# Performance work log

Measured on AMD Instinct MI355X. Metric: run time of the kernel, lower is better.

The kernel has to match this reference:

```python
import jax, jax.numpy as jnp
import numpy as np

BS, N, W, R = 32, 2048, 128, 8
EPS = 1e-8

def setup_inputs() -> dict:
    key = jax.random.key(0)
    ks = jax.random.split(key, 16)
    memory = jax.random.normal(ks[0], (N, W), jnp.float32)
    usage_vector = jax.random.uniform(ks[1], (BS, N), jnp.float32)
    p = jax.random.uniform(ks[2], (BS, N), jnp.float32)
    precedence_weighting = p / p.sum(1, keepdims=True)
    temporal_memory_linkage = jax.random.uniform(ks[3], (BS, N, N), jnp.float32) / N
    lr = jax.random.uniform(ks[4], (BS, N, R), jnp.float32)
    last_read_weightings = lr / lr.sum(1, keepdims=True)
    read_keys = jax.random.normal(ks[5], (BS, W, R), jnp.float32)
    read_strengths = 1.0 + 4.0 * jax.random.uniform(ks[6], (BS, R), jnp.float32)
    write_key = jax.random.normal(ks[7], (BS, W), jnp.float32)
    write_strength = 1.0 + 4.0 * jax.random.uniform(ks[8], (BS, 1), jnp.float32)
    erase_vector = jax.random.uniform(ks[9], (BS, W), jnp.float32)
    write_vector = jax.random.normal(ks[10], (BS, W), jnp.float32)
    free_gates = jax.random.uniform(ks[11], (BS, R), jnp.float32)
    allocation_gate = jax.random.uniform(ks[12], (BS, 1), jnp.float32)
    write_gate = jax.random.uniform(ks[13], (BS, 1), jnp.float32)
    rm = jax.random.uniform(ks[14], (BS, R, 3), jnp.float32)
    read_modes = rm / rm.sum(-1, keepdims=True)
    return dict(memory=memory, usage_vector=usage_vector,
                precedence_weighting=precedence_weighting,
                temporal_memory_linkage=temporal_memory_linkage,
                last_read_weightings=last_read_weightings,
                read_keys=read_keys, read_strengths=read_strengths,
                write_key=write_key, write_strength=write_strength,
                erase_vector=erase_vector, write_vector=write_vector,
                free_gates=free_gates, allocation_gate=allocation_gate,
                write_gate=write_gate, read_modes=read_modes)


def reference(memory, usage_vector, precedence_weighting, temporal_memory_linkage,
              last_read_weightings, read_keys, read_strengths, write_key,
              write_strength, erase_vector, write_vector, free_gates,
              allocation_gate, write_gate, read_modes):
    bs = usage_vector.shape[0]
    # --- allocation weighting (sort + cumprod + gather), from previous usage ---
    sorted_u = jnp.sort(usage_vector, axis=1)                 # (bs,N)
    indices = jnp.argsort(usage_vector, axis=1)               # (bs,N)
    cp = jnp.cumprod(sorted_u, axis=1)
    cp = jnp.concatenate([jnp.ones((bs, 1), usage_vector.dtype), cp], axis=1)[:, :-1]
    alloc_sorted = (1.0 - sorted_u) * cp
    # faithful to torch.gather(aw, 1, indices)
    alloc = jnp.take_along_axis(alloc_sorted, indices, axis=1)  # (bs,N)
    # --- write content weighting (cosine sim + softmax) ---
    innerprod = write_key @ memory.T                          # (bs,N)
    memnorm = jnp.linalg.norm(memory, axis=1)                 # (N,)
    writenorm = jnp.linalg.norm(write_key, axis=1)            # (bs,)
    sim = innerprod / jnp.clip(memnorm[None, :] * writenorm[:, None], EPS)
    cw = jax.nn.softmax(sim * write_strength, axis=1)         # (bs,N)
    # --- write weighting ---
    ww = write_gate * (allocation_gate * alloc + (1.0 - allocation_gate) * cw)  # (bs,N)
    # --- memory retention + usage update ---
    psi = jnp.prod(1.0 - last_read_weightings * free_gates[:, None, :], axis=2)  # (bs,N)
    usage_new = (usage_vector + ww - usage_vector * ww) * psi
    # --- write to memory (erase then add, mean over batch) ---
    erase_outer = ww[:, :, None] * erase_vector[:, None, :]   # (bs,N,W)
    add_outer = ww[:, :, None] * write_vector[:, None, :]     # (bs,N,W)
    memory_new = jnp.mean(memory[None] * (1.0 - erase_outer) + add_outer, axis=0)  # (N,W)
    # --- temporal linkage update (uses previous precedence) ---
    ww_i = ww[:, :, None]                                     # (bs,N,1)
    ww_j = ww[:, None, :]                                     # (bs,1,N)
    L_new = (1.0 - ww_j - ww_i) * temporal_memory_linkage + ww_i * precedence_weighting[:, None, :]
    # --- precedence update ---
    prec_new = (1.0 - ww.sum(1, keepdims=True)) * precedence_weighting + ww
    # --- forward / backward weightings ---
    bw = jnp.matmul(L_new, last_read_weightings)              # (bs,N,R)
    fw = jnp.matmul(jnp.swapaxes(L_new, 1, 2), last_read_weightings)  # (bs,N,R)
    # --- read content weighting ---
    innerprod_r = jnp.einsum('nw,bwr->bnr', memory_new, read_keys)    # (bs,N,R)
    mem_norm = jnp.linalg.norm(memory_new, axis=1)            # (N,)
    read_norm = jnp.linalg.norm(read_keys, axis=1)            # (bs,R)
    sim_r = innerprod_r / jnp.clip(mem_norm[None, :, None] * read_norm[:, None, :], EPS)
    cr = jax.nn.softmax(sim_r * read_strengths[:, None, :], axis=1)   # (bs,N,R)
    # --- combine with read modes: stack order [backward, content, forward] ---
    all_w = jnp.stack([bw, cr, fw], axis=1)                   # (bs,3,N,R)
    read_weightings = jnp.einsum('bknr,brk->bnr', all_w, read_modes)  # (bs,N,R)
    # --- read memory ---
    read_vectors = jnp.einsum('nw,bnr->bwr', memory_new, read_weightings)  # (bs,W,R)
    return read_vectors
```

## Files before the change

kernel.cpp:

```cpp
#include <hip/hip_runtime.h>

#define BS 32
#define Nn 2048
#define Ww 128
#define Rr 8
#define EPSF 1e-8f

#define TI   128
#define NT   16
#define WCH  32
#define NCHL 32

#define OFF_WW      0
#define OFF_MEMNEW  (OFF_WW + BS*Nn)
#define OFF_MEMNORM (OFF_MEMNEW + Nn*Ww)
#define OFF_CR      (OFF_MEMNORM + Nn)
#define OFF_M2      (OFF_CR + BS*Nn*Rr)
#define OFF_O1      (OFF_M2 + BS*Nn*16)
#define OFF_C12     (OFF_O1 + 2*BS*Nn*16)
#define OFF_PART    (OFF_C12 + BS*16)
#define OFF_SIM     (OFF_PART + NT*BS*Nn*16)

__device__ __forceinline__ void gload_lds16(const void* g, void* l) {
    __builtin_amdgcn_global_load_lds((const __attribute__((address_space(1))) void*)g,
                                     (__attribute__((address_space(3))) void*)l, 16, 0, 0);
}

#define FMA16(ACC, LV, M0, M1, M2V, M3) \
    ACC[0]  += (LV)*(M0).x;  ACC[1]  += (LV)*(M0).y;  ACC[2]  += (LV)*(M0).z;  ACC[3]  += (LV)*(M0).w; \
    ACC[4]  += (LV)*(M1).x;  ACC[5]  += (LV)*(M1).y;  ACC[6]  += (LV)*(M1).z;  ACC[7]  += (LV)*(M1).w; \
    ACC[8]  += (LV)*(M2V).x; ACC[9]  += (LV)*(M2V).y; ACC[10] += (LV)*(M2V).z; ACC[11] += (LV)*(M2V).w; \
    ACC[12] += (LV)*(M3).x;  ACC[13] += (LV)*(M3).y;  ACC[14] += (LV)*(M3).z;  ACC[15] += (LV)*(M3).w;

__global__ __launch_bounds__(256) void k_sim(const float* __restrict__ mem,
    const float* __restrict__ wkey, const float* __restrict__ wstr,
    float* __restrict__ simg)
{
    __shared__ float sWK[Ww];
    const int b = blockIdx.x >> 3, sl = blockIdx.x & 7;
    const int tx = threadIdx.x;
    if (tx < Ww) sWK[tx] = wkey[b*Ww + tx];
    __syncthreads();
    float wn2 = 0.f;
    #pragma unroll
    for (int w = 0; w < Ww; w += 4) {
        float4 k4 = *(const float4*)(&sWK[w]);
        wn2 += k4.x*k4.x + k4.y*k4.y + k4.z*k4.z + k4.w*k4.w;
    }
    const float wn = sqrtf(wn2);
    const float st = wstr[b];
    const int n = sl*256 + tx;
    const float* mrow = mem + (size_t)n*Ww;
    float dot = 0.f, m2 = 0.f;
    #pragma unroll
    for (int w = 0; w < Ww; w += 4) {
        float4 m4 = *(const float4*)(mrow + w);
        float4 k4 = *(const float4*)(&sWK[w]);
        dot += m4.x*k4.x + m4.y*k4.y + m4.z*k4.z + m4.w*k4.w;
        m2  += m4.x*m4.x + m4.y*m4.y + m4.z*m4.z + m4.w*m4.w;
    }
    float denom = fmaxf(sqrtf(m2)*wn, EPSF);
    simg[b*Nn + n] = dot / denom * st;
}

__global__ __launch_bounds__(512) void k_front(const float* __restrict__ usage,
    const float* __restrict__ simg, const float* __restrict__ agate,
    const float* __restrict__ wgate, const float* __restrict__ lrw,
    const float* __restrict__ prec, float* __restrict__ ww_out,
    float* __restrict__ M2, float* __restrict__ c12)
{
    __shared__ unsigned long long sk[Nn];
    __shared__ float sAll[Nn];
    __shared__ float sSim[Nn];
    __shared__ float sRed[512];
    __shared__ float sQ[64];
    __shared__ float sC[8][16];
    const int b = blockIdx.x, tx = threadIdx.x;

    #pragma unroll
    for (int m = 0; m < 4; ++m) {
        int i = m*512 + tx;
        sk[i] = ((unsigned long long)__float_as_uint(usage[b*Nn + i]) << 32) | (unsigned)i;
    }
    __syncthreads();
    for (int k = 2; k <= Nn; k <<= 1) {
        for (int j = k >> 1; j > 0; j >>= 1) {
            #pragma unroll
            for (int m = 0; m < 4; ++m) {
                int i = m*512 + tx;
                int ixj = i ^ j;
                if (ixj > i) {
                    bool up = ((i & k) == 0);
                    unsigned long long a = sk[i], c = sk[ixj];
                    if (up ? (a > c) : (a < c)) { sk[i] = c; sk[ixj] = a; }
                }
            }
            __syncthreads();
        }
    }
    {
        float p = 1.f;
        #pragma unroll
        for (int e = 0; e < 4; ++e)
            p *= __uint_as_float((unsigned)(sk[tx*4 + e] >> 32));
        sRed[tx] = p;
        __syncthreads();
        if (tx < 64) {
            float q = 1.f;
            #pragma unroll
            for (int e = 0; e < 8; ++e) q *= sRed[tx*8 + e];
            sQ[tx] = q;
        }
        __syncthreads();
        if (tx == 0) {
            float run = 1.f;
            for (int s = 0; s < 64; ++s) { float t = sQ[s]; sQ[s] = run; run *= t; }
        }
        __syncthreads();
        float run = sQ[tx >> 3];
        for (int s = (tx & ~7); s < tx; ++s) run *= sRed[s];
        #pragma unroll
        for (int e = 0; e < 4; ++e) {
            float v = __uint_as_float((unsigned)(sk[tx*4 + e] >> 32));
            sAll[tx*4 + e] = (1.f - v) * run;
            run *= v;
        }
    }
    #pragma unroll
    for (int m = 0; m < 4; ++m) {
        int n = m*512 + tx;
        sSim[n] = simg[b*Nn + n];
    }
    __syncthreads();
    float allocr[4];
    #pragma unroll
    for (int m = 0; m < 4; ++m) {
        int i = m*512 + tx;
        allocr[m] = sAll[(unsigned)(sk[i] & 0xffffffffu)];
    }
    float lm = -3.402823466e38f;
    #pragma unroll
    for (int m = 0; m < 4; ++m) lm = fmaxf(lm, sSim[m*512 + tx]);
    sRed[tx] = lm; __syncthreads();
    for (int s = 256; s > 0; s >>= 1) { if (tx < s) sRed[tx] = fmaxf(sRed[tx], sRed[tx+s]); __syncthreads(); }
    float mx = sRed[0]; __syncthreads();
    float ls = 0.f;
    #pragma unroll
    for (int m = 0; m < 4; ++m) ls += expf(sSim[m*512 + tx] - mx);
    sRed[tx] = ls; __syncthreads();
    for (int s = 256; s > 0; s >>= 1) { if (tx < s) sRed[tx] += sRed[tx+s]; __syncthreads(); }
    float inv = 1.f / sRed[0];
    float ag = agate[b], wg = wgate[b];
    float wwr[4];
    #pragma unroll
    for (int m = 0; m < 4; ++m) {
        int n = m*512 + tx;
        float cw = expf(sSim[n] - mx) * inv;
        wwr[m] = wg * (ag * allocr[m] + (1.f - ag) * cw);
        ww_out[b*Nn + n] = wwr[m];
    }

    float c1p[8] = {0,0,0,0,0,0,0,0};
    float c2p[8] = {0,0,0,0,0,0,0,0};
    #pragma unroll
    for (int m = 0; m < 4; ++m) {
        int j = m*512 + tx;
        size_t jb = (size_t)b*Nn + j;
        float4 a  = *(const float4*)(lrw + jb*Rr);
        float4 b4 = *(const float4*)(lrw + jb*Rr + 4);
        float w = wwr[m], pv = prec[jb];
        float* dst = M2 + jb*16;
        ((float4*)dst)[0] = a;
        ((float4*)dst)[1] = b4;
        ((float4*)dst)[2] = make_float4(a.x*w,  a.y*w,  a.z*w,  a.w*w);
        ((float4*)dst)[3] = make_float4(b4.x*w, b4.y*w, b4.z*w, b4.w*w);
        c1p[0] += pv*a.x;  c1p[1] += pv*a.y;  c1p[2] += pv*a.z;  c1p[3] += pv*a.w;
        c1p[4] += pv*b4.x; c1p[5] += pv*b4.y; c1p[6] += pv*b4.z; c1p[7] += pv*b4.w;
        c2p[0] += w*a.x;   c2p[1] += w*a.y;   c2p[2] += w*a.z;   c2p[3] += w*a.w;
        c2p[4] += w*b4.x;  c2p[5] += w*b4.y;  c2p[6] += w*b4.z;  c2p[7] += w*b4.w;
    }
    #pragma unroll
    for (int r = 0; r < 8; ++r) {
        float v1 = c1p[r], v2 = c2p[r];
        #pragma unroll
        for (int m = 1; m < 64; m <<= 1) { v1 += __shfl_xor(v1, m); v2 += __shfl_xor(v2, m); }
        c1p[r] = v1; c2p[r] = v2;
    }
    int wv = tx >> 6;
    if ((tx & 63) == 0) {
        #pragma unroll
        for (int r = 0; r < 8; ++r) { sC[wv][r] = c1p[r]; sC[wv][8+r] = c2p[r]; }
    }
    __syncthreads();
    if (tx < 16) {
        float s = 0.f;
        #pragma unroll
        for (int w8 = 0; w8 < 8; ++w8) s += sC[w8][tx];
        c12[b*16 + tx] = s;
    }
}

__global__ void k_memnew(const float* __restrict__ mem, const float* __restrict__ ww,
                         const float* __restrict__ erasev, const float* __restrict__ wvec,
                         float* __restrict__ memnew, float* __restrict__ memnorm)
{
    __shared__ float s_red[2][Ww];
    int tx = threadIdx.x;
    int h = tx >> 7, w = tx & 127;
    int n = blockIdx.x * 2 + h;
    float accE = 0.f, accA = 0.f;
    for (int b = 0; b < BS; ++b) {
        float wwv = ww[b*Nn + n];
        accE += wwv * erasev[b*Ww + w];
        accA += wwv * wvec[b*Ww + w];
    }
    const float inv = 1.f / (float)BS;
    float m = mem[(size_t)n*Ww + w];
    float outv = m * (1.f - accE*inv) + accA*inv;
    memnew[(size_t)n*Ww + w] = outv;
    s_red[h][w] = outv*outv;
    __syncthreads();
    for (int s = 64; s > 0; s >>= 1) { if (w < s) s_red[h][w] += s_red[h][w+s]; __syncthreads(); }
    if (w == 0) memnorm[n] = sqrtf(s_red[h][0]);
}

__global__ void k_cr(const float* __restrict__ memnew, const float* __restrict__ memnorm,
                     const float* __restrict__ rkeys, const float* __restrict__ rstr,
                     float* __restrict__ cr)
{
    __shared__ float s_key[Ww];
    __shared__ float s_sim[Nn];
    __shared__ float s_red[256];
    int b = blockIdx.x >> 3, r = blockIdx.x & 7;
    int tx = threadIdx.x;
    if (tx < Ww) s_key[tx] = rkeys[(b*Ww + tx)*Rr + r];
    __syncthreads();
    float kn2 = 0.f;
    #pragma unroll
    for (int w = 0; w < Ww; ++w) { float k = s_key[w]; kn2 += k*k; }
    float kn = sqrtf(kn2);
    float st = rstr[b*Rr + r];
    for (int n = tx; n < Nn; n += 256) {
        const float* mrow = memnew + (size_t)n*Ww;
        float dot = 0.f;
        for (int w = 0; w < Ww; w += 4) {
            float4 m4 = *(const float4*)(mrow + w);
            float4 k4 = *(const float4*)(&s_key[w]);
            dot += m4.x*k4.x + m4.y*k4.y + m4.z*k4.z + m4.w*k4.w;
        }
        float denom = fmaxf(memnorm[n]*kn, EPSF);
        s_sim[n] = dot / denom * st;
    }
    __syncthreads();
    float lm = -3.402823466e38f;
    for (int n = tx; n < Nn; n += 256) lm = fmaxf(lm, s_sim[n]);
    s_red[tx] = lm; __syncthreads();
    for (int s = 128; s > 0; s >>= 1) { if (tx < s) s_red[tx] = fmaxf(s_red[tx], s_red[tx+s]); __syncthreads(); }
    float mx = s_red[0]; __syncthreads();
    float ls = 0.f;
    for (int n = tx; n < Nn; n += 256) ls += expf(s_sim[n] - mx);
    s_red[tx] = ls; __syncthreads();
    for (int s = 128; s > 0; s >>= 1) { if (tx < s) s_red[tx] += s_red[tx+s]; __syncthreads(); }
    float inv = 1.f / s_red[0];
    for (int n = tx; n < Nn; n += 256)
        cr[((size_t)b*Nn + n)*Rr + r] = expf(s_sim[n] - mx) * inv;
}

__global__ __launch_bounds__(256, 2) void k_link(const float* __restrict__ L,
    const float* __restrict__ M2g, float* __restrict__ O1g, float* __restrict__ partg)
{
    __shared__ float4 sTile[2][TI*8];
    __shared__ float4 sM2c[2][WCH*4];
    __shared__ float4 sM2r[TI*4];
    __shared__ float4 sCmb[4*4*33];

    const int b     = blockIdx.x >> 5;
    const int rem   = blockIdx.x & 31;
    const int tile  = rem >> 1;
    const int chalf = rem & 1;
    const int i0    = tile * TI;
    const int j0    = chalf * (Nn/2);
    const int tx    = threadIdx.x;
    const int wv    = tx >> 6;

    const float* Lb  = L + (size_t)b*Nn*Nn;
    const float* M2b = M2g + (size_t)b*Nn*16;

    const int iq  = tx & 63;
    const int cq  = tx & 7;
    const int chq = (tx >> 3) & 3;
    const int rh  = tx >> 5;

    auto stageTile = [&](int t) {
        const int tb = t & 1;
        const int jc = j0 + t*WCH;
        #pragma unroll
        for (int k = 0; k < 4; ++k) {
            int s = k*256 + tx;
            int i = s >> 3, cp = s & 7;
            const float* src = Lb + (size_t)(i0 + i)*Nn + jc + 4*(cp ^ (i & 7));
            gload_lds16(src, &sTile[tb][k*256 + (wv<<6)]);
        }
        if (wv >= 2) {
            int s = tx - 128;
            const float* src = M2b + (size_t)(jc + (s>>2))*16 + (s&3)*4;
            gload_lds16(src, &sM2c[tb][(wv-2)<<6]);
        }
    };

    #pragma unroll
    for (int k = 0; k < 2; ++k) {
        int s = k*256 + tx;
        const float* src = M2b + (size_t)(i0 + (s>>2))*16 + (s&3)*4;
        gload_lds16(src, &sM2r[k*256 + (wv<<6)]);
    }
    stageTile(0);

    float P0[16], P1[16];
    #pragma unroll
    for (int c = 0; c < 16; ++c) { P0[c] = 0.f; P1[c] = 0.f; }

    #pragma unroll 1
    for (int t = 0; t < NCHL; ++t) {
        const int tb = t & 1;
        __builtin_amdgcn_s_barrier();
        __builtin_amdgcn_sched_barrier(0);
        if (t+1 < NCHL) stageTile(t+1);
        if (t == NCHL-1) {
            asm volatile("s_waitcnt vmcnt(0)" ::: "memory");
        } else if (t == 0) {
            if (wv < 2) asm volatile("s_waitcnt vmcnt(4)" ::: "memory");
            else        asm volatile("s_waitcnt vmcnt(5)" ::: "memory");
        } else {
            asm volatile("s_waitcnt vmcnt(5)" ::: "memory");
        }
        __builtin_amdgcn_sched_barrier(0);
        __builtin_amdgcn_s_barrier();
        __builtin_amdgcn_sched_barrier(0);

        const float4* tileb = sTile[tb];
        const float4* m2cb  = sM2c[tb];

        #pragma unroll
        for (int jo = 0; jo < 2; ++jo) {
            const int jj4 = wv*2 + jo;
            float4 Lv0 = tileb[iq*8      + (jj4 ^ (iq & 7))];
            float4 Lv1 = tileb[(iq+64)*8 + (jj4 ^ (iq & 7))];
            #pragma unroll
            for (int jj = 0; jj < 4; ++jj) {
                const int j = jj4*4 + jj;
                float4 m0 = m2cb[j*4+0], m1 = m2cb[j*4+1], m2v = m2cb[j*4+2], m3 = m2cb[j*4+3];
                float a0 = (jj==0)?Lv0.x:(jj==1)?Lv0.y:(jj==2)?Lv0.z:Lv0.w;
                float a1 = (jj==0)?Lv1.x:(jj==1)?Lv1.y:(jj==2)?Lv1.z:Lv1.w;
                FMA16(P0, a0, m0, m1, m2v, m3)
                FMA16(P1, a1, m0, m1, m2v, m3)
            }
        }

        {
            float acc[4][4];
            #pragma unroll
            for (int c = 0; c < 4; ++c)
                #pragma unroll
                for (int e = 0; e < 4; ++e) acc[c][e] = 0.f;
            #pragma unroll 8
            for (int ii = 0; ii < 16; ++ii) {
                int i = rh*16 + ii;
                float4 Lq = tileb[i*8 + (cq ^ (i & 7))];
                float4 m  = sM2r[i*4 + chq];
                acc[0][0] += Lq.x*m.x; acc[0][1] += Lq.x*m.y; acc[0][2] += Lq.x*m.z; acc[0][3] += Lq.x*m.w;
                acc[1][0] += Lq.y*m.x; acc[1][1] += Lq.y*m.y; acc[1][2] += Lq.y*m.z; acc[1][3] += Lq.y*m.w;
                acc[2][0] += Lq.z*m.x; acc[2][1] += Lq.z*m.y; acc[2][2] += Lq.z*m.z; acc[2][3] += Lq.z*m.w;
                acc[3][0] += Lq.w*m.x; acc[3][1] += Lq.w*m.y; acc[3][2] += Lq.w*m.z; acc[3][3] += Lq.w*m.w;
            }
            #pragma unroll
            for (int c = 0; c < 4; ++c)
                #pragma unroll
                for (int e = 0; e < 4; ++e)
                    acc[c][e] += __shfl_xor(acc[c][e], 32);
            if ((tx & 32) == 0) {
                int slot = tx & 31;
                #pragma unroll
                for (int c = 0; c < 4; ++c)
                    sCmb[wv*132 + c*33 + slot] =
                        make_float4(acc[c][0], acc[c][1], acc[c][2], acc[c][3]);
            }
        }
        asm volatile("s_waitcnt lgkmcnt(0)" ::: "memory");
        __builtin_amdgcn_sched_barrier(0);
        __builtin_amdgcn_s_barrier();
        __builtin_amdgcn_sched_barrier(0);

        if (tx < 128) {
            int col = tx >> 2, cq4 = tx & 3;
            int slot = cq4*8 + (col >> 2), c = col & 3;
            float4 a0 = sCmb[0*132 + c*33 + slot];
            float4 a1 = sCmb[1*132 + c*33 + slot];
            float4 a2 = sCmb[2*132 + c*33 + slot];
            float4 a3 = sCmb[3*132 + c*33 + slot];
            float4 s;
            s.x = a0.x+a1.x+a2.x+a3.x; s.y = a0.y+a1.y+a2.y+a3.y;
            s.z = a0.z+a1.z+a2.z+a3.z; s.w = a0.w+a1.w+a2.w+a3.w;
            float* pbase = partg + (((size_t)(tile*BS + b))*Nn + j0 + t*WCH)*16;
            ((float4*)pbase)[tx] = s;
        }
    }

    __syncthreads();
    float4* planes4 = (float4*)sTile;
    #pragma unroll
    for (int c4 = 0; c4 < 4; ++c4) {
        planes4[wv*512 + c4*128 + iq]      = make_float4(P0[c4*4],P0[c4*4+1],P0[c4*4+2],P0[c4*4+3]);
        planes4[wv*512 + c4*128 + iq + 64] = make_float4(P1[c4*4],P1[c4*4+1],P1[c4*4+2],P1[c4*4+3]);
    }
    __syncthreads();
    float4* obase = (float4*)(O1g + ((size_t)(chalf*BS + b)*Nn + i0)*16);
    #pragma unroll
    for (int e = 0; e < 2; ++e) {
        int f = e*256 + tx;
        int row = f >> 2, c4 = f & 3;
        float4 s0 = planes4[0*512 + c4*128 + row];
        float4 s1 = planes4[1*512 + c4*128 + row];
        float4 s2 = planes4[2*512 + c4*128 + row];
        float4 s3 = planes4[3*512 + c4*128 + row];
        float4 s;
        s.x = s0.x+s1.x+s2.x+s3.x; s.y = s0.y+s1.y+s2.y+s3.y;
        s.z = s0.z+s1.z+s2.z+s3.z; s.w = s0.w+s1.w+s2.w+s3.w;
        obase[f] = s;
    }
}

__global__ void k_read(const float* __restrict__ memnew, const float* __restrict__ O1g,
                       const float* __restrict__ partg, const float* __restrict__ cr,
                       const float* __restrict__ ww, const float* __restrict__ prec,
                       const float* __restrict__ c12, const float* __restrict__ rmodes,
                       float* __restrict__ out)
{
    __shared__ float s_o2[256][17];
    __shared__ float s_o1[256][17];
    __shared__ float s_rw[256][Rr];
    __shared__ float s_rm[Rr*3];
    __shared__ float s_c12[16];
    __shared__ float s_part[2][Ww][Rr];
    int b = blockIdx.x >> 3, slice = blockIdx.x & 7;
    int n0 = slice * 256;
    int tx = threadIdx.x;
    if (tx < Rr*3) s_rm[tx] = rmodes[b*Rr*3 + tx];
    if (tx < 16)   s_c12[tx] = c12[b*16 + tx];
    __syncthreads();
    #pragma unroll
    for (int k = 0; k < 4; ++k) {
        int f = k*256 + tx;
        int n = f >> 2, c4 = f & 3;
        float4 acc = make_float4(0.f,0.f,0.f,0.f);
        for (int t = 0; t < NT; ++t) {
            float4 v = ((const float4*)(partg + ((size_t)(t*BS + b)*Nn + n0)*16))[f];
            acc.x += v.x; acc.y += v.y; acc.z += v.z; acc.w += v.w;
        }
        s_o2[n][c4*4+0] = acc.x; s_o2[n][c4*4+1] = acc.y;
        s_o2[n][c4*4+2] = acc.z; s_o2[n][c4*4+3] = acc.w;
        float4 o1a = ((const float4*)(O1g + ((size_t)(0*BS + b)*Nn + n0)*16))[f];
        float4 o1b = ((const float4*)(O1g + ((size_t)(1*BS + b)*Nn + n0)*16))[f];
        s_o1[n][c4*4+0] = o1a.x+o1b.x; s_o1[n][c4*4+1] = o1a.y+o1b.y;
        s_o1[n][c4*4+2] = o1a.z+o1b.z; s_o1[n][c4*4+3] = o1a.w+o1b.w;
    }
    __syncthreads();
    {
        int n = n0 + tx;
        float wwv = ww[b*Nn + n], pv = prec[b*Nn + n];
        float4 cr0 = *(const float4*)(cr + ((size_t)b*Nn + n)*Rr);
        float4 cr1 = *(const float4*)(cr + ((size_t)b*Nn + n)*Rr + 4);
        float crv[8] = {cr0.x,cr0.y,cr0.z,cr0.w,cr1.x,cr1.y,cr1.z,cr1.w};
        #pragma unroll
        for (int r = 0; r < 8; ++r) {
            float bwv = (1.f - wwv)*s_o1[tx][r] - s_o1[tx][8+r] + wwv*s_c12[r];
            float fwv = (1.f - wwv)*s_o2[tx][r] - s_o2[tx][8+r] + pv*s_c12[8+r];
            s_rw[tx][r] = bwv*s_rm[r*3+0] + crv[r]*s_rm[r*3+1] + fwv*s_rm[r*3+2];
        }
    }
    __syncthreads();
    int w = tx & 127, hh = tx >> 7;
    float acc[Rr] = {0,0,0,0,0,0,0,0};
    for (int nl = hh*128; nl < hh*128 + 128; ++nl) {
        float mval = memnew[(size_t)(n0 + nl)*Ww + w];
        #pragma unroll
        for (int r = 0; r < Rr; ++r) acc[r] += mval * s_rw[nl][r];
    }
    #pragma unroll
    for (int r = 0; r < Rr; ++r) s_part[hh][w][r] = acc[r];
    __syncthreads();
    if (hh == 0) {
        #pragma unroll
        for (int r = 0; r < Rr; ++r)
            unsafeAtomicAdd(&out[(w*Rr + r) + b*Ww*Rr], s_part[0][w][r] + s_part[1][w][r]);
    }
}

extern "C" void kernel_launch(void* const* d_in, const int* in_sizes, int n_in,
                              void* d_out, int out_size, void* d_ws, size_t ws_size,
                              hipStream_t stream) {
    const float* mem    = (const float*)d_in[0];
    const float* usage  = (const float*)d_in[1];
    const float* prec   = (const float*)d_in[2];
    const float* Lmat   = (const float*)d_in[3];
    const float* lrw    = (const float*)d_in[4];
    const float* rkeys  = (const float*)d_in[5];
    const float* rstr   = (const float*)d_in[6];
    const float* wkey   = (const float*)d_in[7];
    const float* wstr   = (const float*)d_in[8];
    const float* erasev = (const float*)d_in[9];
    const float* wvec   = (const float*)d_in[10];
    const float* agate  = (const float*)d_in[12];
    const float* wgate  = (const float*)d_in[13];
    const float* rmodes = (const float*)d_in[14];

    float* ws       = (float*)d_ws;
    float* ww_      = ws + OFF_WW;
    float* memnew_  = ws + OFF_MEMNEW;
    float* memnorm_ = ws + OFF_MEMNORM;
    float* cr_      = ws + OFF_CR;
    float* M2_      = ws + OFF_M2;
    float* O1_      = ws + OFF_O1;
    float* c12_     = ws + OFF_C12;
    float* part_    = ws + OFF_PART;
    float* sim_     = ws + OFF_SIM;
    float* outf     = (float*)d_out;

    hipMemsetAsync(outf, 0, (size_t)out_size*sizeof(float), stream);

    k_sim   <<<BS*8,    256, 0, stream>>>(mem, wkey, wstr, sim_);
    k_front <<<BS,      512, 0, stream>>>(usage, sim_, agate, wgate, lrw, prec, ww_, M2_, c12_);
    k_memnew<<<Nn/2,    256, 0, stream>>>(mem, ww_, erasev, wvec, memnew_, memnorm_);
    k_cr    <<<BS*Rr,   256, 0, stream>>>(memnew_, memnorm_, rkeys, rstr, cr_);
    k_link  <<<BS*NT*2, 256, 0, stream>>>(Lmat, M2_, O1_, part_);
    k_read  <<<BS*8,    256, 0, stream>>>(memnew_, O1_, part_, cr_, ww_, prec, c12_, rmodes, outf);
}
```

Before: 401.0 us.

## Split read content weighting into batched dot kernel and separate softmax kernel

The read-content kernel used one block per (batch, read head), and each block streamed all of memnew to compute a single dot product per row. It is split into two kernels. The first computes all 8 read-head dots per memory row in one pass, with the keys held in shared memory, and writes the scaled similarities. The second runs the per-head softmax in place over that buffer. This cuts memnew reads eightfold and raises arithmetic per load, at the cost of one extra launch and a round trip of the similarity buffer through global memory.

```diff
diff --git a/kernel.cpp b/kernel.cpp
--- a/kernel.cpp
+++ b/kernel.cpp
@@ -224,33 +224,60 @@
     if (w == 0) memnorm[n] = sqrtf(s_red[h][0]);
 }
 
-__global__ void k_cr(const float* __restrict__ memnew, const float* __restrict__ memnorm,
-                     const float* __restrict__ rkeys, const float* __restrict__ rstr,
-                     float* __restrict__ cr)
-{
-    __shared__ float s_key[Ww];
+__global__ __launch_bounds__(256) void k_crdot(const float* __restrict__ memnew,
+    const float* __restrict__ memnorm, const float* __restrict__ rkeys,
+    const float* __restrict__ rstr, float* __restrict__ crbuf)
+{
+    __shared__ float sK[Ww][Rr];
+    __shared__ float sKn[Rr];
+    __shared__ float sSt[Rr];
+    const int b = blockIdx.x >> 3, sl = blockIdx.x & 7;
+    const int tx = threadIdx.x;
+    for (int k = tx; k < Ww*Rr; k += 256) {
+        int w = k >> 3, r = k & 7;
+        sK[w][r] = rkeys[((size_t)b*Ww + w)*Rr + r];
+    }
+    if (tx < Rr) sSt[tx] = rstr[b*Rr + tx];
+    __syncthreads();
+    if (tx < Rr) {
+        float kn2 = 0.f;
+        for (int w = 0; w < Ww; ++w) { float k = sK[w][tx]; kn2 += k*k; }
+        sKn[tx] = sqrtf(kn2);
+    }
+    __syncthreads();
+    const int n = sl*256 + tx;
+    const float* mrow = memnew + (size_t)n*Ww;
+    float dot[8] = {0,0,0,0,0,0,0,0};
+    #pragma unroll 4
+    for (int w = 0; w < Ww; w += 4) {
+        float4 m4 = *(const float4*)(mrow + w);
+        #pragma unroll
+        for (int l = 0; l < 4; ++l) {
+            float mv = (l==0)?m4.x:(l==1)?m4.y:(l==2)?m4.z:m4.w;
+            float4 k0 = *(const float4*)(&sK[w+l][0]);
+            float4 k1 = *(const float4*)(&sK[w+l][4]);
+            dot[0] += mv*k0.x; dot[1] += mv*k0.y; dot[2] += mv*k0.z; dot[3] += mv*k0.w;
+            dot[4] += mv*k1.x; dot[5] += mv*k1.y; dot[6] += mv*k1.z; dot[7] += mv*k1.w;
+        }
+    }
+    const float mn = memnorm[n];
+    float simv[8];
+    #pragma unroll
+    for (int r = 0; r < 8; ++r)
+        simv[r] = dot[r] / fmaxf(mn*sKn[r], EPSF) * sSt[r];
+    float* dst = crbuf + ((size_t)b*Nn + n)*Rr;
+    ((float4*)dst)[0] = make_float4(simv[0], simv[1], simv[2], simv[3]);
+    ((float4*)dst)[1] = make_float4(simv[4], simv[5], simv[6], simv[7]);
+}
+
+__global__ __launch_bounds__(256) void k_crsm(float* __restrict__ crbuf)
+{
     __shared__ float s_sim[Nn];
     __shared__ float s_red[256];
-    int b = blockIdx.x >> 3, r = blockIdx.x & 7;
-    int tx = threadIdx.x;
-    if (tx < Ww) s_key[tx] = rkeys[(b*Ww + tx)*Rr + r];
-    __syncthreads();
-    float kn2 = 0.f;
-    #pragma unroll
-    for (int w = 0; w < Ww; ++w) { float k = s_key[w]; kn2 += k*k; }
-    float kn = sqrtf(kn2);
-    float st = rstr[b*Rr + r];
-    for (int n = tx; n < Nn; n += 256) {
-        const float* mrow = memnew + (size_t)n*Ww;
-        float dot = 0.f;
-        for (int w = 0; w < Ww; w += 4) {
-            float4 m4 = *(const float4*)(mrow + w);
-            float4 k4 = *(const float4*)(&s_key[w]);
-            dot += m4.x*k4.x + m4.y*k4.y + m4.z*k4.z + m4.w*k4.w;
-        }
-        float denom = fmaxf(memnorm[n]*kn, EPSF);
-        s_sim[n] = dot / denom * st;
-    }
+    const int b = blockIdx.x >> 3, r = blockIdx.x & 7;
+    const int tx = threadIdx.x;
+    for (int n = tx; n < Nn; n += 256)
+        s_sim[n] = crbuf[((size_t)b*Nn + n)*Rr + r];
     __syncthreads();
     float lm = -3.402823466e38f;
     for (int n = tx; n < Nn; n += 256) lm = fmaxf(lm, s_sim[n]);
@@ -263,7 +290,7 @@
     for (int s = 128; s > 0; s >>= 1) { if (tx < s) s_red[tx] += s_red[tx+s]; __syncthreads(); }
     float inv = 1.f / s_red[0];
     for (int n = tx; n < Nn; n += 256)
-        cr[((size_t)b*Nn + n)*Rr + r] = expf(s_sim[n] - mx) * inv;
+        crbuf[((size_t)b*Nn + n)*Rr + r] = expf(s_sim[n] - mx) * inv;
 }
 
 __global__ __launch_bounds__(256, 2) void k_link(const float* __restrict__ L,
@@ -531,7 +558,8 @@
     k_sim   <<<BS*8,    256, 0, stream>>>(mem, wkey, wstr, sim_);
     k_front <<<BS,      512, 0, stream>>>(usage, sim_, agate, wgate, lrw, prec, ww_, M2_, c12_);
     k_memnew<<<Nn/2,    256, 0, stream>>>(mem, ww_, erasev, wvec, memnew_, memnorm_);
-    k_cr    <<<BS*Rr,   256, 0, stream>>>(memnew_, memnorm_, rkeys, rstr, cr_);
+    k_crdot <<<BS*8,    256, 0, stream>>>(memnew_, memnorm_, rkeys, rstr, cr_);
+    k_crsm  <<<BS*Rr,   256, 0, stream>>>(cr_);
     k_link  <<<BS*NT*2, 256, 0, stream>>>(Lmat, M2_, O1_, part_);
     k_read  <<<BS*8,    256, 0, stream>>>(memnew_, O1_, part_, cr_, ww_, prec, c12_, rmodes, outf);
 }
```

New measurement: 366.1 us, median of 2. 8.7% less time.
